# Kernel optimization log

Hardware: AMD Instinct MI355X
Metric: run time of the kernel (lower is better)

## Reference

```python
import jax, jax.numpy as jnp
import numpy as np

LN_EPS = 1e-5
LOCAL_SIZE = 256
N_HEAD, D_HEAD = 16, 64


def layer_norm_c(x):
    # layer norm over channel dim (axis=1), no affine params (matches F.layer_norm(x.T,(d,)).T)
    m = jnp.mean(x, axis=1, keepdims=True)
    v = jnp.var(x, axis=1, keepdims=True)
    return (x - m) / jnp.sqrt(v + LN_EPS)


def rel_shift(x):
    # x: [b, n, q, k] -> Transformer-XL relative shift
    b, n, q, k = x.shape
    x = jnp.pad(x, ((0, 0), (0, 0), (0, 0), (1, 0)))
    return x.reshape(b, n, k + 1, q)[:, :, 1:].reshape(b, n, q, k)


def setup_inputs() -> dict:
    key = jax.random.key(0)
    ks = jax.random.split(key, 14)
    bsz, d_model, qlen, mlen = 4, 1024, 512, 512
    klen = qlen + mlen
    d_inner = 4096
    s = lambda k, shape, sc=0.05: jax.random.normal(k, shape, dtype=jnp.float32) * sc
    return {
        "z1ss": jax.random.normal(ks[0], (bsz, d_model, qlen), dtype=jnp.float32),
        "uss": jax.random.normal(ks[1], (bsz, 3 * d_model, klen), dtype=jnp.float32) * 0.1,
        "z0": jax.random.normal(ks[2], (bsz, d_model, mlen), dtype=jnp.float32),
        "pos_emb": jax.random.normal(ks[3], (1, d_model, klen), dtype=jnp.float32),
        "qkv_w": s(ks[4], (3 * d_model, d_model)),
        "r_w": s(ks[5], (d_model, d_model)),
        "r_w_bias": s(ks[6], (N_HEAD, D_HEAD)),
        "r_r_bias": s(ks[7], (N_HEAD, D_HEAD)),
        "o_w": s(ks[8], (d_model, d_model)),
        "o_b": s(ks[9], (d_model,)),
        "ff1_w": s(ks[10], (d_inner, d_model)),
        "ff1_b": s(ks[11], (d_inner,)),
        "ff2_w": s(ks[12], (d_model, d_inner)),
        "ff2_b": s(ks[13], (d_model,)),
    }


def reference(z1ss, uss, z0, pos_emb, qkv_w, r_w, r_w_bias, r_r_bias, o_w, o_b,
              ff1_w, ff1_b, ff2_w, ff2_b):
    bsz, d_model, qlen = z1ss.shape
    mlen = z0.shape[2]
    n_head, d_head = N_HEAD, D_HEAD
    scale = 1.0 / d_head ** 0.5

    # ---- self-attention (post-lnorm path) ----
    cat = jnp.concatenate([z0, z1ss], axis=-1)              # [b, d, klen]
    klen = cat.shape[2]
    w_heads = jnp.einsum('od,bdk->bok', qkv_w, cat) + uss   # [b, 3d, klen]
    r_head_k = jnp.einsum('od,dk->ok', r_w, pos_emb[0])     # [d, rlen]
    rlen = r_head_k.shape[1]

    w_head_q, w_head_k, w_head_v = jnp.split(w_heads, 3, axis=1)
    w_head_q = w_head_q[:, :, -qlen:]
    w_head_q = w_head_q.reshape(bsz, n_head, d_head, qlen)
    w_head_k = w_head_k.reshape(bsz, n_head, d_head, klen)
    w_head_v = w_head_v.reshape(bsz, n_head, d_head, klen)
    r_head_k = r_head_k.reshape(n_head, d_head, rlen)

    rw_q = w_head_q + r_w_bias[:, :, None]                  # [b,n,d,q]
    AC = jnp.einsum('bndi,bndj->bnij', rw_q, w_head_k)      # [b,n,q,k]
    rr_q = w_head_q + r_r_bias[:, :, None]
    BD = rel_shift(jnp.einsum('bndi,ndj->bnij', rr_q, r_head_k))
    attn_score = (AC + BD) * scale

    local_size = LOCAL_SIZE if LOCAL_SIZE else 1000
    i = jnp.arange(qlen)[:, None]
    j = jnp.arange(klen)[None, :]
    mask = (j > i + mlen) | (j <= i + mlen - local_size)    # causal + local window
    attn_score = jnp.where(mask[None, None], -jnp.inf, attn_score)

    attn_prob = jax.nn.softmax(attn_score, axis=-1)
    attn_vec = jnp.einsum('bnij,bndj->bndi', attn_prob, w_head_v)
    attn_vec = attn_vec.reshape(bsz, n_head * d_head, qlen)
    attn_out = jnp.einsum('od,bdq->boq', o_w, attn_vec) + o_b[None, :, None]
    x = layer_norm_c(attn_out + z1ss)                       # post-lnorm

    # ---- position-wise FF (weight-shared, post-lnorm) ----
    h = jax.nn.relu(jnp.einsum('id,bdq->biq', ff1_w, x) + ff1_b[None, :, None])
    out2 = jnp.einsum('di,biq->bdq', ff2_w, h) + ff2_b[None, :, None]
    return layer_norm_c(out2 + x)
```

## Files before the change

kernel.cpp:

```cpp
#include <hip/hip_runtime.h>
#include <hip/hip_bf16.h>

typedef unsigned short u16;
typedef __attribute__((ext_vector_type(8))) short s8v;
typedef __attribute__((ext_vector_type(4))) short s4v;
typedef __attribute__((ext_vector_type(4))) float f4v;

__device__ __forceinline__ float s2f(u16 s) {
    unsigned int u = ((unsigned int)s) << 16;
    return __builtin_bit_cast(float, u);
}
__device__ __forceinline__ u16 f2s(float f) {
    __hip_bfloat16 h = __float2bfloat16(f);
    return __builtin_bit_cast(u16, h);
}

__device__ __forceinline__ void gl2lds16(const u16* g, u16* l) {
    __builtin_amdgcn_global_load_lds((const __attribute__((address_space(1))) void*)g,
                                     (__attribute__((address_space(3))) void*)l, 16, 0, 0);
}

#define BSZ 4
#define DM 1024
#define QLEN 512
#define MLEN 512
#define KLEN 1024
#define DI 4096
#define NH 16
#define DH 64
#define WIN 256

__global__ __launch_bounds__(256) void conv_w(const float* __restrict__ src,
                                              u16* __restrict__ dst, int n4) {
    int i = blockIdx.x * 256 + threadIdx.x;
    if (i < n4) {
        f4v v = *(const f4v*)&src[(size_t)i * 4];
        s4v o;
#pragma unroll
        for (int k = 0; k < 4; ++k) o[k] = (short)f2s(v[k]);
        *(s4v*)&dst[(size_t)i * 4] = o;
    }
}

__global__ __launch_bounds__(256) void trans_f2b(
    const float* __restrict__ src, long sS, int ldS, int colOff,
    u16* __restrict__ dst, long sD, int ldD, int rowOff)
{
    __shared__ float tile[32][33];
    int b = blockIdx.z;
    int t0 = blockIdx.x * 32, f0 = blockIdx.y * 32;
    int tx = threadIdx.x, ty = threadIdx.y;
#pragma unroll
    for (int p = 0; p < 4; ++p)
        tile[ty + 8 * p][tx] = src[(size_t)b * sS + (size_t)(f0 + ty + 8 * p) * ldS + colOff + t0 + tx];
    __syncthreads();
#pragma unroll
    for (int p = 0; p < 4; ++p)
        dst[(size_t)b * sD + (size_t)(rowOff + t0 + ty + 8 * p) * ldD + f0 + tx] = f2s(tile[tx][ty + 8 * p]);
}

__global__ __launch_bounds__(256) void trans_b2f(
    const u16* __restrict__ src, long sS, int ldS,
    float* __restrict__ dst, long sD, int ldD)
{
    __shared__ float tile[32][33];
    int b = blockIdx.z;
    int t0 = blockIdx.x * 32, f0 = blockIdx.y * 32;
    int tx = threadIdx.x, ty = threadIdx.y;
#pragma unroll
    for (int p = 0; p < 4; ++p)
        tile[ty + 8 * p][tx] = s2f(src[(size_t)b * sS + (size_t)(f0 + ty + 8 * p) * ldS + t0 + tx]);
    __syncthreads();
#pragma unroll
    for (int p = 0; p < 4; ++p)
        dst[(size_t)b * sD + (size_t)(t0 + ty + 8 * p) * ldD + f0 + tx] = tile[tx][ty + 8 * p];
}

template<int BN, int SPLIT>
__global__ __launch_bounds__(256) void gemm_bt(
    const u16* __restrict__ A,
    const u16* __restrict__ B,
    u16* __restrict__ C,
    float* __restrict__ fOut,
    int M, int K,
    const float* __restrict__ bias,
    const float* __restrict__ uss,
    int relu,
    long pstride)
{
    constexpr int BM = 128, BK = 64;
    constexpr int MI = (BN == 128) ? 4 : 2;
    constexpr int NI = 4;
    const int n0 = blockIdx.x * BN, m0 = blockIdx.y * BM;
    const int Ks = K / SPLIT;
    const int kbeg = blockIdx.z * Ks;
    __shared__ __align__(16) u16 As[BM * BK];
    __shared__ __align__(16) u16 Bs[BN * BK];
    const int tid = threadIdx.x, lane = tid & 63, wv = tid >> 6;
    const int l15 = lane & 15, quad = lane >> 4;
    const int wm = (BN == 128) ? (wv >> 1) * 64 : wv * 32;
    const int wn = (BN == 128) ? (wv & 1) * 64 : 0;
    f4v acc[MI][NI] = {};
    for (int kk = kbeg; kk < kbeg + Ks; kk += BK) {
        __syncthreads();
#pragma unroll
        for (int p = 0; p < (BM * 8) / 256; ++p) {
            int c = p * 256 + tid, r = c >> 3, q = c & 7, qs = q ^ (r & 7);
            gl2lds16(&A[(size_t)(m0 + r) * K + kk + qs * 8], &As[c * 8]);
        }
#pragma unroll
        for (int p = 0; p < (BN * 8) / 256; ++p) {
            int c = p * 256 + tid, r = c >> 3, q = c & 7, qs = q ^ (r & 7);
            gl2lds16(&B[(size_t)(n0 + r) * K + kk + qs * 8], &Bs[c * 8]);
        }
        __syncthreads();
#pragma unroll
        for (int k0 = 0; k0 < BK; k0 += 32) {
            s8v af[MI], bf[NI];
#pragma unroll
            for (int mi = 0; mi < MI; ++mi) {
                int r = wm + mi * 16 + l15;
                af[mi] = *(const s8v*)&As[r * BK + ((((k0 >> 3) + quad) ^ (r & 7)) << 3)];
            }
#pragma unroll
            for (int ni = 0; ni < NI; ++ni) {
                int r = wn + ni * 16 + l15;
                bf[ni] = *(const s8v*)&Bs[r * BK + ((((k0 >> 3) + quad) ^ (r & 7)) << 3)];
            }
#pragma unroll
            for (int mi = 0; mi < MI; ++mi)
#pragma unroll
                for (int ni = 0; ni < NI; ++ni)
                    acc[mi][ni] = __builtin_amdgcn_mfma_f32_16x16x32_bf16(af[mi], bf[ni], acc[mi][ni], 0, 0, 0);
        }
    }
    if (SPLIT > 1) {
        float* base = fOut + (long)blockIdx.z * pstride;
#pragma unroll
        for (int mi = 0; mi < MI; ++mi) {
            int m = m0 + wm + mi * 16 + quad * 4;
#pragma unroll
            for (int ni = 0; ni < NI; ++ni) {
                int n = n0 + wn + ni * 16 + l15;
                *(f4v*)&base[(size_t)n * M + m] = acc[mi][ni];
            }
        }
    } else {
#pragma unroll
        for (int mi = 0; mi < MI; ++mi) {
            int m = m0 + wm + mi * 16 + quad * 4;
            float bv[4] = {0.f, 0.f, 0.f, 0.f};
            if (bias) {
#pragma unroll
                for (int r2 = 0; r2 < 4; ++r2) bv[r2] = bias[m + r2];
            }
#pragma unroll
            for (int ni = 0; ni < NI; ++ni) {
                int n = n0 + wn + ni * 16 + l15;
                float o[4];
#pragma unroll
                for (int r2 = 0; r2 < 4; ++r2) o[r2] = acc[mi][ni][r2] + bv[r2];
                if (uss) {
                    int b = n >> 10, t = n & 1023;
#pragma unroll
                    for (int r2 = 0; r2 < 4; ++r2)
                        o[r2] += uss[((size_t)b * 3072 + m + r2) * 1024 + t];
                }
                if (relu) {
#pragma unroll
                    for (int r2 = 0; r2 < 4; ++r2) o[r2] = fmaxf(o[r2], 0.f);
                }
                s4v st;
#pragma unroll
                for (int r2 = 0; r2 < 4; ++r2) st[r2] = (short)f2s(o[r2]);
                *(s4v*)&C[(size_t)n * M + m] = st;
            }
        }
    }
}

#define QT 16
#define KT 272
#define KROW 72
#define VROW 280
#define SROW 272
#define PROW 280
__global__ __launch_bounds__(256) void attn_mfma(
    const u16* __restrict__ WHT,
    const u16* __restrict__ RT,
    const float* __restrict__ rwb, const float* __restrict__ rrb,
    u16* __restrict__ avT)
{
    __shared__ __align__(16) u16  sKV[KT * KROW];
    __shared__ __align__(16) float sS[QT * SROW];
    __shared__ __align__(16) u16  sP[QT * PROW];

    const int qt = blockIdx.x, n = blockIdx.y, b = blockIdx.z;
    const int i0 = qt * QT, j0 = i0 + WIN + 1;
    const int tid = threadIdx.x, lane = tid & 63, wv = tid >> 6;
    const int l15 = lane & 15, quad = lane >> 4;
    const u16* W = WHT + (size_t)b * KLEN * (3 * DM);

    s8v qac[2], qbd[2];
    {
        int qrow = MLEN + i0 + l15;
#pragma unroll
        for (int kc = 0; kc < 2; ++kc) {
            int col = n * DH + kc * 32 + quad * 8;
            s8v qv = *(const s8v*)&W[(size_t)qrow * (3 * DM) + col];
            s8v a, c;
#pragma unroll
            for (int e = 0; e < 8; ++e) {
                float qf = s2f((u16)qv[e]);
                a[e] = (short)f2s(qf + rwb[col + e]);
                c[e] = (short)f2s(qf + rrb[col + e]);
            }
            qac[kc] = a; qbd[kc] = c;
        }
    }

    for (int t = tid; t < KT * 8; t += 256) {
        int r = t >> 3, q = t & 7;
        int j = j0 + r; if (j > KLEN - 1) j = KLEN - 1;
        *(s8v*)&sKV[r * KROW + q * 8] = *(const s8v*)&W[(size_t)j * (3 * DM) + DM + n * DH + q * 8];
    }
    for (int t = tid; t < QT * SROW; t += 256) sS[t] = -1e30f;
    __syncthreads();

#pragma unroll
    for (int cc = 0; cc < 4; ++cc) {
        int ci = wv + cc * 4;
        f4v acc = {};
#pragma unroll
        for (int kc = 0; kc < 2; ++kc) {
            s8v bf = *(const s8v*)&RT[(size_t)(ci * 16 + l15) * DM + n * DH + kc * 32 + quad * 8];
            acc = __builtin_amdgcn_mfma_f32_16x16x32_bf16(qbd[kc], bf, acc, 0, 0, 0);
        }
#pragma unroll
        for (int r2 = 0; r2 < 4; ++r2) {
            int qi = quad * 4 + r2;
            sS[qi * SROW + qi + ci * 16 + l15] = acc[r2];
        }
    }
    __syncthreads();

    for (int ci = wv; ci < 17; ci += 4) {
        f4v acc = {};
#pragma unroll
        for (int kc = 0; kc < 2; ++kc) {
            s8v bf = *(const s8v*)&sKV[(ci * 16 + l15) * KROW + kc * 32 + quad * 8];
            acc = __builtin_amdgcn_mfma_f32_16x16x32_bf16(qac[kc], bf, acc, 0, 0, 0);
        }
#pragma unroll
        for (int r2 = 0; r2 < 4; ++r2) {
            int qi = quad * 4 + r2;
            sS[qi * SROW + ci * 16 + l15] += acc[r2];
        }
    }
    __syncthreads();

    {
        int q = tid >> 5, r0 = tid & 31;
        for (int k = 0; k < 9; ++k) {
            int r = r0 + 32 * k;
            if (r < KT) {
                int j = j0 + r; if (j > KLEN - 1) j = KLEN - 1;
                s8v vv = *(const s8v*)&W[(size_t)j * (3 * DM) + 2 * DM + n * DH + q * 8];
#pragma unroll
                for (int e = 0; e < 8; ++e)
                    sKV[(q * 8 + e) * VROW + r] = (u16)vv[e];
            }
        }
    }

    {
        int g = tid >> 4, l = tid & 15;
        float vals[17], mx = -1e30f;
#pragma unroll
        for (int k = 0; k < 17; ++k) {
            float s = sS[g * SROW + l + 16 * k] * 0.125f;
            vals[k] = s; mx = fmaxf(mx, s);
        }
#pragma unroll
        for (int d = 1; d < 16; d <<= 1) mx = fmaxf(mx, __shfl_xor(mx, d, 16));
        float sum = 0.f;
#pragma unroll
        for (int k = 0; k < 17; ++k) { vals[k] = __expf(vals[k] - mx); sum += vals[k]; }
#pragma unroll
        for (int d = 1; d < 16; d <<= 1) sum += __shfl_xor(sum, d, 16);
        float inv = 1.f / sum;
#pragma unroll
        for (int k = 0; k < 17; ++k) sP[g * PROW + l + 16 * k] = f2s(vals[k] * inv);
    }
    __syncthreads();

    f4v o = {};
    for (int kc = 0; kc < 9; ++kc) {
        s8v a = {}, bb = {};
        if (kc < 8) {
            a  = *(const s8v*)&sP[l15 * PROW + kc * 32 + quad * 8];
            bb = *(const s8v*)&sKV[(wv * 16 + l15) * VROW + kc * 32 + quad * 8];
        } else if (quad < 2) {
            a  = *(const s8v*)&sP[l15 * PROW + 256 + quad * 8];
            bb = *(const s8v*)&sKV[(wv * 16 + l15) * VROW + 256 + quad * 8];
        }
        o = __builtin_amdgcn_mfma_f32_16x16x32_bf16(a, bb, o, 0, 0, 0);
    }
#pragma unroll
    for (int r2 = 0; r2 < 4; ++r2) {
        int qi = quad * 4 + r2;
        avT[((size_t)b * QLEN + i0 + qi) * DM + n * DH + wv * 16 + l15] = f2s(o[r2]);
    }
}

__global__ __launch_bounds__(256) void ln_f(
    const float* __restrict__ P, long pstride, int nparts,
    const float* __restrict__ bias,
    const u16* __restrict__ res, int resMode, u16* __restrict__ out)
{
    int n = blockIdx.x, tid = threadIdx.x;
    int lane = tid & 63, wv = tid >> 6;
    int f = tid * 4;
    int rrow = resMode ? (((n >> 9) * 2 + 1) * 512 + (n & 511)) : n;
    f4v pv = *(const f4v*)&P[(size_t)n * DM + f];
    for (int p = 1; p < nparts; ++p) {
        const float* Pp = P + (long)p * pstride;
        pv += *(const f4v*)&Pp[(size_t)n * DM + f];
    }
    s4v rv = *(const s4v*)&res[(size_t)rrow * DM + f];
    f4v bv = *(const f4v*)&bias[f];
    float v[4];
#pragma unroll
    for (int k = 0; k < 4; ++k) v[k] = pv[k] + bv[k] + s2f((u16)rv[k]);
    float s = v[0] + v[1] + v[2] + v[3];
    float ss = v[0] * v[0] + v[1] * v[1] + v[2] * v[2] + v[3] * v[3];
#pragma unroll
    for (int d = 1; d < 64; d <<= 1) {
        s += __shfl_xor(s, d, 64);
        ss += __shfl_xor(ss, d, 64);
    }
    __shared__ float ps[4], pss[4];
    if (lane == 0) { ps[wv] = s; pss[wv] = ss; }
    __syncthreads();
    float S = ps[0] + ps[1] + ps[2] + ps[3];
    float SS = pss[0] + pss[1] + pss[2] + pss[3];
    float m = S * (1.f / DM);
    float var = SS * (1.f / DM) - m * m;
    float inv = rsqrtf(fmaxf(var, 0.f) + 1e-5f);
    s4v st;
#pragma unroll
    for (int k = 0; k < 4; ++k) st[k] = (short)f2s((v[k] - m) * inv);
    *(s4v*)&out[(size_t)n * DM + f] = st;
}

extern "C" void kernel_launch(void* const* d_in, const int* in_sizes, int n_in,
                              void* d_out, int out_size, void* d_ws, size_t ws_size,
                              hipStream_t stream) {
    const float* z1ss  = (const float*)d_in[0];
    const float* uss   = (const float*)d_in[1];
    const float* z0    = (const float*)d_in[2];
    const float* pos   = (const float*)d_in[3];
    const float* qkv_w = (const float*)d_in[4];
    const float* r_w   = (const float*)d_in[5];
    const float* rwb   = (const float*)d_in[6];
    const float* rrb   = (const float*)d_in[7];
    const float* o_w   = (const float*)d_in[8];
    const float* o_b   = (const float*)d_in[9];
    const float* ff1_w = (const float*)d_in[10];
    const float* ff1_b = (const float*)d_in[11];
    const float* ff2_w = (const float*)d_in[12];
    const float* ff2_b = (const float*)d_in[13];

    u16* ws = (u16*)d_ws;
    u16* wQ   = ws;
    u16* wR   = ws + 3145728;
    u16* wO   = ws + 4194304;
    u16* wF1  = ws + 5242880;
    u16* wF2  = ws + 9437184;
    u16* catT = ws + 13631488;
    u16* whT  = ws + 17825792;
    u16* posT = ws + 30408704;
    u16* rT   = ws + 30670848;
    u16* avT  = ws + 30932992;
    u16* xT   = ws + 33030144;
    float* pref = (float*)(ws + 35127296);
    u16* hT   = whT;
    u16* outT = catT;

    float* part1 = (float*)d_ws;
    long pstr = part1 - pref;

    dim3 tblk(32, 8);

    conv_w<<<3072, 256, 0, stream>>>(qkv_w, wQ, 786432);
    conv_w<<<1024, 256, 0, stream>>>(r_w,   wR, 262144);
    conv_w<<<1024, 256, 0, stream>>>(o_w,   wO, 262144);
    conv_w<<<4096, 256, 0, stream>>>(ff1_w, wF1, 1048576);
    conv_w<<<4096, 256, 0, stream>>>(ff2_w, wF2, 1048576);

    trans_f2b<<<dim3(16, 32, BSZ), tblk, 0, stream>>>(z0, (long)DM * MLEN, MLEN, 0,
                                                      catT, (long)KLEN * DM, DM, 0);
    trans_f2b<<<dim3(16, 32, BSZ), tblk, 0, stream>>>(z1ss, (long)DM * QLEN, QLEN, 0,
                                                      catT, (long)KLEN * DM, DM, MLEN);
    trans_f2b<<<dim3(8, 32, 1), tblk, 0, stream>>>(pos, 0, KLEN, KLEN - WIN,
                                                   posT, 0, DM, 0);

    gemm_bt<128, 1><<<dim3(32, 24, 1), 256, 0, stream>>>(
        wQ, catT, whT, nullptr, 3 * DM, DM, nullptr, uss, 0, 0);

    gemm_bt<64, 1><<<dim3(4, 8, 1), 256, 0, stream>>>(
        wR, posT, rT, nullptr, DM, DM, nullptr, nullptr, 0, 0);

    attn_mfma<<<dim3(QLEN / QT, NH, BSZ), 256, 0, stream>>>(whT, rT, rwb, rrb, avT);

    gemm_bt<64, 2><<<dim3(32, 8, 2), 256, 0, stream>>>(
        wO, avT, nullptr, pref, DM, DM, nullptr, nullptr, 0, pstr);

    ln_f<<<2048, 256, 0, stream>>>(pref, pstr, 2, o_b, catT, 1, xT);

    gemm_bt<128, 1><<<dim3(16, 32, 1), 256, 0, stream>>>(
        wF1, xT, hT, nullptr, DI, DM, ff1_b, nullptr, 1, 0);

    gemm_bt<64, 2><<<dim3(32, 8, 2), 256, 0, stream>>>(
        wF2, hT, nullptr, pref, DM, DI, nullptr, nullptr, 0, pstr);

    ln_f<<<2048, 256, 0, stream>>>(pref, pstr, 2, ff2_b, xT, 0, outT);

    trans_b2f<<<dim3(32, 16, BSZ), tblk, 0, stream>>>(outT, (long)QLEN * DM, DM,
                                                      (float*)d_out, (long)DM * QLEN, QLEN);
}
```

Baseline: 367.0 us.

## Merge weight conversions, split uss add into transpose kernel, shrink GEMM tiles

The five fp32-to-bf16 weight conversion launches are merged into one kernel that picks source and destination by index range. The uss residual add is taken out of the QKV GEMM epilogue and moved into a separate transpose-and-add kernel that reads back and rewrites the bf16 output. The QKV and FF1 GEMMs also drop from 128 to 64 tile width with doubled grids, which gives more blocks. Together these trade fewer launches and more parallelism for an extra pass over the whT buffer and an extra bf16 rounding step.

```diff
diff --git a/kernel.cpp b/kernel.cpp
--- a/kernel.cpp
+++ b/kernel.cpp
@@ -30,16 +30,28 @@
 #define DH 64
 #define WIN 256
 
-__global__ __launch_bounds__(256) void conv_w(const float* __restrict__ src,
-                                              u16* __restrict__ dst, int n4) {
+__global__ __launch_bounds__(256) void conv_w5(
+    const float* __restrict__ s0, const float* __restrict__ s1,
+    const float* __restrict__ s2, const float* __restrict__ s3,
+    const float* __restrict__ s4,
+    u16* __restrict__ d0, u16* __restrict__ d1, u16* __restrict__ d2,
+    u16* __restrict__ d3, u16* __restrict__ d4)
+{
+    const int e0 = 786432, e1 = e0 + 262144, e2 = e1 + 262144,
+              e3 = e2 + 1048576, e4 = e3 + 1048576;
     int i = blockIdx.x * 256 + threadIdx.x;
-    if (i < n4) {
-        f4v v = *(const f4v*)&src[(size_t)i * 4];
-        s4v o;
-#pragma unroll
-        for (int k = 0; k < 4; ++k) o[k] = (short)f2s(v[k]);
-        *(s4v*)&dst[(size_t)i * 4] = o;
-    }
+    const float* s; u16* d; int off;
+    if (i < e0)      { s = s0; d = d0; off = i; }
+    else if (i < e1) { s = s1; d = d1; off = i - e0; }
+    else if (i < e2) { s = s2; d = d2; off = i - e1; }
+    else if (i < e3) { s = s3; d = d3; off = i - e2; }
+    else if (i < e4) { s = s4; d = d4; off = i - e3; }
+    else return;
+    f4v v = *(const f4v*)&s[(size_t)off * 4];
+    s4v o;
+#pragma unroll
+    for (int k = 0; k < 4; ++k) o[k] = (short)f2s(v[k]);
+    *(s4v*)&d[(size_t)off * 4] = o;
 }
 
 __global__ __launch_bounds__(256) void trans_f2b(
@@ -57,6 +69,26 @@
 #pragma unroll
     for (int p = 0; p < 4; ++p)
         dst[(size_t)b * sD + (size_t)(rowOff + t0 + ty + 8 * p) * ldD + f0 + tx] = f2s(tile[tx][ty + 8 * p]);
+}
+
+__global__ __launch_bounds__(256) void trans_add(
+    const float* __restrict__ src, u16* __restrict__ dst)
+{
+    __shared__ float tile[32][33];
+    int b = blockIdx.z;
+    int t0 = blockIdx.x * 32, f0 = blockIdx.y * 32;
+    int tx = threadIdx.x, ty = threadIdx.y;
+    const float* S = src + (size_t)b * 3072 * 1024;
+    u16* D = dst + (size_t)b * 1024 * 3072;
+#pragma unroll
+    for (int p = 0; p < 4; ++p)
+        tile[ty + 8 * p][tx] = S[(size_t)(f0 + ty + 8 * p) * 1024 + t0 + tx];
+    __syncthreads();
+#pragma unroll
+    for (int p = 0; p < 4; ++p) {
+        size_t o = (size_t)(t0 + ty + 8 * p) * 3072 + f0 + tx;
+        D[o] = f2s(s2f(D[o]) + tile[tx][ty + 8 * p]);
+    }
 }
 
 __global__ __launch_bounds__(256) void trans_b2f(
@@ -392,11 +424,8 @@
 
     dim3 tblk(32, 8);
 
-    conv_w<<<3072, 256, 0, stream>>>(qkv_w, wQ, 786432);
-    conv_w<<<1024, 256, 0, stream>>>(r_w,   wR, 262144);
-    conv_w<<<1024, 256, 0, stream>>>(o_w,   wO, 262144);
-    conv_w<<<4096, 256, 0, stream>>>(ff1_w, wF1, 1048576);
-    conv_w<<<4096, 256, 0, stream>>>(ff2_w, wF2, 1048576);
+    conv_w5<<<13312, 256, 0, stream>>>(qkv_w, r_w, o_w, ff1_w, ff2_w,
+                                       wQ, wR, wO, wF1, wF2);
 
     trans_f2b<<<dim3(16, 32, BSZ), tblk, 0, stream>>>(z0, (long)DM * MLEN, MLEN, 0,
                                                       catT, (long)KLEN * DM, DM, 0);
@@ -405,8 +434,10 @@
     trans_f2b<<<dim3(8, 32, 1), tblk, 0, stream>>>(pos, 0, KLEN, KLEN - WIN,
                                                    posT, 0, DM, 0);
 
-    gemm_bt<128, 1><<<dim3(32, 24, 1), 256, 0, stream>>>(
-        wQ, catT, whT, nullptr, 3 * DM, DM, nullptr, uss, 0, 0);
+    gemm_bt<64, 1><<<dim3(64, 24, 1), 256, 0, stream>>>(
+        wQ, catT, whT, nullptr, 3 * DM, DM, nullptr, nullptr, 0, 0);
+
+    trans_add<<<dim3(32, 96, BSZ), tblk, 0, stream>>>(uss, whT);
 
     gemm_bt<64, 1><<<dim3(4, 8, 1), 256, 0, stream>>>(
         wR, posT, rT, nullptr, DM, DM, nullptr, nullptr, 0, 0);
@@ -418,7 +449,7 @@
 
     ln_f<<<2048, 256, 0, stream>>>(pref, pstr, 2, o_b, catT, 1, xT);
 
-    gemm_bt<128, 1><<<dim3(16, 32, 1), 256, 0, stream>>>(
+    gemm_bt<64, 1><<<dim3(32, 32, 1), 256, 0, stream>>>(
         wF1, xT, hT, nullptr, DI, DM, ff1_b, nullptr, 1, 0);
 
     gemm_bt<64, 2><<<dim3(32, 8, 2), 256, 0, stream>>>(
```

Result: no change. 365.1 us (-0.5%).
